# Optimization experiments

Hardware: AMD Instinct MI355X
Metric: run time of the kernel (lower is better)

The kernel has to match this reference:

```python
import jax, jax.numpy as jnp
import numpy as np

N_ATOMS = 512
N_FEATURES = 64
BATCH = 8
BINS = 64
SEG_LEN = 1
LEAKY_SLOPE = 0.01


def _segments(n, length=1):
    # all pairs of segments (i,i+length),(j,j+length), i<j, excluding end1==start2
    n_seg = n - length
    i, j = np.triu_indices(n_seg, k=1)
    seg = np.stack([i, i + length, j, j + length], axis=1)
    return seg[seg[:, 1] != seg[:, 2]].astype(np.int32)


def _nnorm(v):
    return v / jnp.linalg.norm(v, axis=-1, keepdims=True)


def _writhe(segments, xyz):
    # segments: (P,4) int, xyz: (B,N,3) -> (B,P)
    smat = xyz[:, segments]                                  # (B,P,4,3)
    B, P = smat.shape[0], smat.shape[1]
    # displacements r02,r03,r12,r13 (point a in seg1 -> point b in seg2)
    disp = _nnorm((smat[:, :, None, 2:, :] - smat[:, :, :2, None, :]).reshape(B, P, 4, 3))
    idx_a = jnp.array([0, 1, 3, 2])
    idx_b = jnp.array([1, 3, 2, 0])
    crosses = _nnorm(jnp.cross(disp[:, :, idx_a], disp[:, :, idx_b]))
    dots = jnp.clip(jnp.sum(crosses * crosses[:, :, idx_b], axis=-1), -1.0, 1.0)
    omega = jnp.arcsin(dots).sum(-1)                         # (B,P)
    signs = jnp.sign(jnp.sum(
        jnp.cross(_nnorm(smat[:, :, 3] - smat[:, :, 2]), _nnorm(smat[:, :, 1] - smat[:, :, 0]))
        * disp[:, :, 0], axis=-1))
    return omega * signs / (2.0 * jnp.pi)


def _rbf(x, start=-1.0, end=1.0, number=BINS):
    # soft_one_hot_linspace, basis='gaussian', cutoff=False
    values = jnp.linspace(start, end, number, dtype=x.dtype)
    step = values[1] - values[0]
    diff = (x[..., None] - values) / step
    return jnp.exp(-(diff ** 2)) / 1.12


def setup_inputs() -> dict:
    key = jax.random.key(0)
    k = jax.random.split(key, 4)
    seg = jnp.asarray(_segments(N_ATOMS, SEG_LEN))           # (129795,4)
    return {
        "x": jax.random.normal(k[0], (BATCH, N_ATOMS, N_FEATURES), jnp.float32),
        "xyz": jax.random.normal(k[1], (BATCH, N_ATOMS, 3), jnp.float32) * 3.0,
        "segments": seg,
        "W1": jax.random.normal(k[2], (BINS, N_FEATURES), jnp.float32) / np.sqrt(BINS),
        "b1": jnp.zeros((N_FEATURES,), jnp.float32),
        "W2": jax.random.normal(k[3], (N_FEATURES, N_FEATURES), jnp.float32) / np.sqrt(N_FEATURES),
        "b2": jnp.zeros((N_FEATURES,), jnp.float32),
    }


def reference(x, xyz, segments, W1, b1, W2, b2):
    wr = _writhe(segments, xyz)                              # (B,P)
    # bidirectional edges between segment start points
    src = jnp.concatenate([segments[:, 0], segments[:, 2]])  # (E,)
    dst = jnp.concatenate([segments[:, 2], segments[:, 0]])  # (E,)
    wr_e = jnp.concatenate([wr, wr], axis=1)                 # (B,E)
    h = jax.nn.leaky_relu(_rbf(wr_e) @ W1 + b1, LEAKY_SLOPE) # (B,E,F)
    msg = (h @ W2 + b2) * x[:, src]                          # (B,E,F)
    agg = jax.vmap(lambda m: jax.ops.segment_sum(m, dst, num_segments=N_ATOMS))(msg)
    return x + agg                                           # residual update (B,N,F)
```

## Files before the change

kernel.cpp:

```cpp
#include <hip/hip_runtime.h>
#include <hip/hip_bf16.h>
#include <math.h>
#include <stdint.h>

#define N_ATOMS 512
#define NF 64
#define NB 8
#define NBINS 64
#define NSEG 511
#define NTF 8192
#define NSENT 2554
#define ETILES2 254

__device__ __forceinline__ float dot3(float ax, float ay, float az,
                                      float bx, float by, float bz) {
    return fmaf(ax, bx, fmaf(ay, by, az * bz));
}

__device__ __forceinline__ uint16_t bf16_bits(float f) {
    union { __hip_bfloat16 h; uint16_t u; } cv;
    cv.h = __float2bfloat16(f);
    return cv.u;
}

__device__ __forceinline__ float compute_wr(const float* pb, int i, int j) {
    float p0x = pb[3*i+0], p0y = pb[3*i+1], p0z = pb[3*i+2];
    float p1x = pb[3*i+3], p1y = pb[3*i+4], p1z = pb[3*i+5];
    float p2x = pb[3*j+0], p2y = pb[3*j+1], p2z = pb[3*j+2];
    float p3x = pb[3*j+3], p3y = pb[3*j+4], p3z = pb[3*j+5];

    float d0x = p2x-p0x, d0y = p2y-p0y, d0z = p2z-p0z;
    float d1x = p3x-p0x, d1y = p3y-p0y, d1z = p3z-p0z;
    float d2x = p2x-p1x, d2y = p2y-p1y, d2z = p2z-p1z;
    float d3x = p3x-p1x, d3y = p3y-p1y, d3z = p3z-p1z;
    {
        float n0 = rsqrtf(dot3(d0x,d0y,d0z,d0x,d0y,d0z)); d0x*=n0; d0y*=n0; d0z*=n0;
        float n1 = rsqrtf(dot3(d1x,d1y,d1z,d1x,d1y,d1z)); d1x*=n1; d1y*=n1; d1z*=n1;
        float n2 = rsqrtf(dot3(d2x,d2y,d2z,d2x,d2y,d2z)); d2x*=n2; d2y*=n2; d2z*=n2;
        float n3 = rsqrtf(dot3(d3x,d3y,d3z,d3x,d3y,d3z)); d3x*=n3; d3y*=n3; d3z*=n3;
    }
    float c0x = d0y*d1z - d0z*d1y, c0y = d0z*d1x - d0x*d1z, c0z = d0x*d1y - d0y*d1x;
    float c1x = d1y*d3z - d1z*d3y, c1y = d1z*d3x - d1x*d3z, c1z = d1x*d3y - d1y*d3x;
    float c3x = d2y*d0z - d2z*d0y, c3y = d2z*d0x - d2x*d0z, c3z = d2x*d0y - d2y*d0x;
    {
        float n0 = rsqrtf(dot3(c0x,c0y,c0z,c0x,c0y,c0z)); c0x*=n0; c0y*=n0; c0z*=n0;
        float n1 = rsqrtf(dot3(c1x,c1y,c1z,c1x,c1y,c1z)); c1x*=n1; c1y*=n1; c1z*=n1;
        float n3 = rsqrtf(dot3(c3x,c3y,c3z,c3x,c3y,c3z)); c3x*=n3; c3y*=n3; c3z*=n3;
    }
    float t0 = fminf(fmaxf(dot3(c0x,c0y,c0z, c1x,c1y,c1z), -1.f), 1.f);
    float t1 = fminf(fmaxf(dot3(c1x,c1y,c1z, c3x,c3y,c3z), -1.f), 1.f);
    float t3 = fminf(fmaxf(dot3(c3x,c3y,c3z, c0x,c0y,c0z), -1.f), 1.f);
    float omega = asinf(t0) + asinf(t1) + asinf(t3) + 1.5707963267948966f;
    float ex = p3x-p2x, ey = p3y-p2y, ez = p3z-p2z;
    float fx = p1x-p0x, fy = p1y-p0y, fz = p1z-p0z;
    float gx = ey*fz - ez*fy, gy = ez*fx - ex*fz, gz = ex*fy - ey*fx;
    float sgd = dot3(gx,gy,gz, d0x,d0y,d0z);
    float sgn = (sgd > 0.f) ? 1.f : ((sgd < 0.f) ? -1.f : 0.f);
    return omega * sgn * 0.15915494309189535f;
}

__device__ __forceinline__ uint32_t wr_to_off(float w) {
    float tf = (w + 1.0f) * ((float)(NTF - 1) * 0.5f);
    tf = fminf(fmaxf(tf, 0.0f), (float)(NTF - 1));
    int t0 = (int)(tf + 0.5f);
    t0 = (t0 > NTF - 1) ? (NTF - 1) : t0;
    return (uint32_t)t0 << 6;
}

__launch_bounds__(256)
__global__ void prepass(
        const float* __restrict__ xyz, const int* __restrict__ seg,
        const float* __restrict__ W1, const float* __restrict__ b1,
        const float* __restrict__ W2, const float* __restrict__ b2,
        uint16_t* __restrict__ tabh, uint32_t* __restrict__ ta, int P) {
    __shared__ float lds[1536];

    const unsigned bx = blockIdx.x;

    if (bx < NTF / 8) {
        const int widx = threadIdx.x >> 6;
        const int lane = threadIdx.x & 63;
        const int g = bx * 4 + widx;
        const int g2 = g + NTF / 2;

        float tta = ((-1.0f + (2.0f / (float)(NTF - 1)) * (float)g)  + 1.0f) * 31.5f;
        float ttb = ((-1.0f + (2.0f / (float)(NTF - 1)) * (float)g2) + 1.0f) * 31.5f;

        float a0=0.f,a1=0.f,a2=0.f,a3=0.f, e0=0.f,e1=0.f,e2=0.f,e3=0.f;
        #pragma unroll
        for (int k = 0; k < NBINS; k += 4) {
            #pragma unroll
            for (int q = 0; q < 4; ++q) {
                float da = tta - (float)(k + q);
                float db = ttb - (float)(k + q);
                float ra = __expf(-da * da) * 0.8928571428571429f;
                float rb = __expf(-db * db) * 0.8928571428571429f;
                float wv = W1[(k + q) * NF + lane];
                if (q == 0) { a0 = fmaf(ra, wv, a0); e0 = fmaf(rb, wv, e0); }
                if (q == 1) { a1 = fmaf(ra, wv, a1); e1 = fmaf(rb, wv, e1); }
                if (q == 2) { a2 = fmaf(ra, wv, a2); e2 = fmaf(rb, wv, e2); }
                if (q == 3) { a3 = fmaf(ra, wv, a3); e3 = fmaf(rb, wv, e3); }
            }
        }
        float ha = ((a0 + a1) + (a2 + a3)) + b1[lane];
        float hb = ((e0 + e1) + (e2 + e3)) + b1[lane];
        ha = fmaxf(ha, 0.01f * ha);
        hb = fmaxf(hb, 0.01f * hb);
        lds[widx * 64 + lane]       = ha;
        lds[256 + widx * 64 + lane] = hb;
        __syncthreads();

        float m0=0.f,m1=0.f,m2=0.f,m3=0.f, n0=0.f,n1=0.f,n2=0.f,n3=0.f;
        #pragma unroll
        for (int k = 0; k < NF; k += 4) {
            float w0 = W2[(k + 0) * NF + lane];
            float w1v = W2[(k + 1) * NF + lane];
            float w2v = W2[(k + 2) * NF + lane];
            float w3 = W2[(k + 3) * NF + lane];
            m0 = fmaf(lds[widx * 64 + k + 0], w0, m0);
            m1 = fmaf(lds[widx * 64 + k + 1], w1v, m1);
            m2 = fmaf(lds[widx * 64 + k + 2], w2v, m2);
            m3 = fmaf(lds[widx * 64 + k + 3], w3, m3);
            n0 = fmaf(lds[256 + widx * 64 + k + 0], w0, n0);
            n1 = fmaf(lds[256 + widx * 64 + k + 1], w1v, n1);
            n2 = fmaf(lds[256 + widx * 64 + k + 2], w2v, n2);
            n3 = fmaf(lds[256 + widx * 64 + k + 3], w3, n3);
        }
        float ma = ((m0 + m1) + (m2 + m3)) + b2[lane];
        float mb = ((n0 + n1) + (n2 + n3)) + b2[lane];
        tabh[g  * NF + lane] = bf16_bits(ma);
        tabh[g2 * NF + lane] = bf16_bits(mb);
        if (g == 0) tabh[NTF * NF + lane] = 0;
    } else if (bx < NTF / 8 + NB * ETILES2) {
        const int rel = bx - NTF / 8;
        const int b = rel / ETILES2;
        const int tile = rel - b * ETILES2;

        const float* xb = xyz + b * (N_ATOMS * 3);
        #pragma unroll
        for (int k = 0; k < 6; ++k)
            lds[k * 256 + threadIdx.x] = xb[k * 256 + threadIdx.x];
        __syncthreads();

        #pragma unroll
        for (int q = 0; q < 2; ++q) {
            const int e = tile * 512 + q * 256 + threadIdx.x;
            if (e < P) {
                int4 sv = ((const int4*)seg)[e];
                const int i = sv.x;
                const int j = sv.z;
                uint32_t u = wr_to_off(compute_wr(lds, i, j));
                ta[(b << 18) + (i << 9) + j] = u;
                ta[(b << 18) + (j << 9) + i] = u;
            }
        }
    } else {
        const int idx = (bx - (NTF / 8 + NB * ETILES2)) * 256 + threadIdx.x;
        if (idx < NB * NSENT) {
            const int b = idx / NSENT;
            const int k = idx - b * NSENT;
            int d, s;
            if      (k < 512)  { d = k;        s = k;     }
            else if (k < 1023) { d = k - 512;  s = d + 1; }
            else if (k < 1534) { s = k - 1023; d = s + 1; }
            else if (k < 2044) { d = k - 1534; s = NSEG;  }
            else               { s = k - 2044; d = NSEG;  }
            ta[(b << 18) + (d << 9) + s] = (uint32_t)NTF << 6;
        }
    }
}

__launch_bounds__(1024, 8)
__global__ void agg15(
        const float* __restrict__ x, const uint32_t* __restrict__ ta,
        const uint16_t* __restrict__ tabh, float* __restrict__ out) {
    __shared__ float xs[16384];

    const int tid  = threadIdx.x;
    const int widx = tid >> 6;
    const int lane = tid & 63;
    const int fl   = lane & 31;
    const int hw   = lane >> 5;
    const int h    = widx >> 3;
    const int r    = widx & 7;
    const int ht   = tid & 511;
    const int bid  = blockIdx.x;
    const int b    = bid >> 6;
    const int dst  = ((bid & 63) << 3) + r;

    const float* xb = x + ((size_t)b << 15);
    const uint32_t* tarow = ta + ((size_t)b << 18) + ((size_t)dst << 9);

    {
        const float* xsrc = xb + ((h * 4) << 12);
        float* xdst = xs + (h << 12);
        #pragma unroll
        for (int k = 0; k < 8; ++k)
            xdst[k * 512 + ht] = xsrc[k * 512 + ht];
    }

    const int xoffl = (hw << 6) + (fl << 1);
    const int feidx = fl << 1;

    float accL = 0.0f, accH = 0.0f;
    #pragma unroll
    for (int p = 0; p < 4; ++p) {
        const int c = h * 4 + p;
        const int tavc = (int)tarow[(c << 6) + lane];

        __syncthreads();

        if (p < 3) {
            const float* xsrc = xb + ((c + 1) << 12);
            float* xdst = xs + ((((p + 1) & 1) << 13) + (h << 12));
            #pragma unroll
            for (int k = 0; k < 8; ++k)
                xdst[k * 512 + ht] = xsrc[k * 512 + ht];
        }

        const float* xc = xs + (((p & 1) << 13) + (h << 12)) + xoffl;
        #pragma unroll
        for (int s4 = 0; s4 < 32; s4 += 4) {
            uint32_t mw[4];
            #pragma unroll
            for (int q = 0; q < 4; ++q) {
                const int s = s4 + q;
                const uint32_t o0 =
                    (uint32_t)__builtin_amdgcn_readlane(tavc, 2 * s);
                const uint32_t o1 =
                    (uint32_t)__builtin_amdgcn_readlane(tavc, 2 * s + 1);
                const uint32_t osel = hw ? o1 : o0;
                mw[q] = *(const uint32_t*)(tabh + osel + feidx);
            }
            #pragma unroll
            for (int q = 0; q < 4; ++q) {
                const int s = s4 + q;
                const float mlo = __uint_as_float(mw[q] << 16);
                const float mhi = __uint_as_float(mw[q] & 0xffff0000u);
                const float2 xv = *(const float2*)(xc + (s << 7));
                accL = fmaf(mlo, xv.x, accL);
                accH = fmaf(mhi, xv.y, accH);
            }
        }
    }
    accL += __shfl_xor(accL, 32);
    accH += __shfl_xor(accH, 32);

    __syncthreads();
    if (h == 1 && hw == 0) {
        xs[(r << 6) + feidx]     = accL;
        xs[(r << 6) + feidx + 1] = accH;
    }
    __syncthreads();
    if (h == 0 && hw == 0) {
        const float2 prev = *(const float2*)&xs[(r << 6) + feidx];
        const float2 xv   = *(const float2*)(xb + (dst << 6) + feidx);
        float2 res;
        res.x = xv.x + accL + prev.x;
        res.y = xv.y + accH + prev.y;
        *(float2*)(out + ((size_t)b << 15) + (dst << 6) + feidx) = res;
    }
}


__global__ void init_out_kernel(const float* __restrict__ x, float* __restrict__ out, int n) {
    int idx = blockIdx.x * blockDim.x + threadIdx.x;
    if (idx < n) out[idx] = x[idx];
}

__device__ __forceinline__ void compute_m(
        const float* __restrict__ pb, int i, int j,
        const float* __restrict__ W1, const float* __restrict__ b1,
        const float* __restrict__ W2, const float* __restrict__ b2,
        float* __restrict__ mout) {
    float wr = compute_wr(pb, i, j);
    float acc_[NBINS];
    {
        float tt = (wr + 1.0f) * 31.5f;
        #pragma unroll
        for (int k = 0; k < NBINS; ++k) {
            float d = tt - (float)k;
            acc_[k] = __expf(-d * d) * 0.8928571428571429f;
        }
    }
    float h_[NF];
    #pragma unroll
    for (int f = 0; f < NF; ++f) h_[f] = b1[f];
    #pragma unroll
    for (int k = 0; k < NBINS; ++k) {
        float r = acc_[k];
        #pragma unroll
        for (int f = 0; f < NF; ++f) h_[f] = fmaf(r, W1[k * NF + f], h_[f]);
    }
    #pragma unroll
    for (int f = 0; f < NF; ++f) h_[f] = fmaxf(h_[f], 0.01f * h_[f]);
    #pragma unroll
    for (int f = 0; f < NF; ++f) acc_[f] = b2[f];
    #pragma unroll
    for (int k = 0; k < NF; ++k) {
        float hk = h_[k];
        #pragma unroll
        for (int f = 0; f < NF; ++f) acc_[f] = fmaf(hk, W2[k * NF + f], acc_[f]);
    }
    #pragma unroll
    for (int f = 0; f < NF; ++f) mout[f] = acc_[f];
}

__launch_bounds__(256, 2)
__global__ void writhe_msg_atomic_kernel(
        const float* __restrict__ x, const float* __restrict__ xyz,
        const int* __restrict__ seg,
        const float* __restrict__ W1, const float* __restrict__ b1,
        const float* __restrict__ W2, const float* __restrict__ b2,
        float* __restrict__ out, int P, int n_tiles) {
    __shared__ __hip_bfloat16 lds_m[4][64 * 65];
    __shared__ int lds_i[4][64];
    __shared__ int lds_j[4][64];

    const int widx = threadIdx.x >> 6;
    const int lane = threadIdx.x & 63;
    const int wave_g = blockIdx.x * 4 + widx;
    const int b = wave_g / n_tiles;
    const int tile = wave_g - b * n_tiles;
    const int bc = (b < NB) ? b : 0;
    const int e = tile * 64 + lane;
    const bool valid = (b < NB) && (e < P);

    int4 sv = valid ? ((const int4*)seg)[e] : make_int4(0, 1, 2, 3);
    const int i = sv.x;
    const int j = sv.z;

    float m[NF];
    compute_m(xyz + bc * (N_ATOMS * 3), i, j, W1, b1, W2, b2, m);

    const float scale = valid ? 1.0f : 0.0f;
    #pragma unroll
    for (int f = 0; f < NF; ++f)
        lds_m[widx][lane * 65 + f] = __float2bfloat16(m[f] * scale);
    lds_i[widx][lane] = i;
    lds_j[widx][lane] = j;
    __syncthreads();

    const float* xb = x + bc * (N_ATOMS * NF);
    float* ob = out + bc * (N_ATOMS * NF);
    int cur_i = lds_i[widx][0];
    float acc_i = 0.0f;
    for (int ee = 0; ee < 64; ++ee) {
        int ie = lds_i[widx][ee];
        int je = lds_j[widx][ee];
        float mv = __bfloat162float(lds_m[widx][ee * 65 + lane]);
        float xi = xb[ie * NF + lane];
        float xj = xb[je * NF + lane];
        atomicAdd(&ob[je * NF + lane], mv * xi);
        if (ie != cur_i) {
            atomicAdd(&ob[cur_i * NF + lane], acc_i);
            acc_i = 0.0f;
            cur_i = ie;
        }
        acc_i = fmaf(mv, xj, acc_i);
    }
    atomicAdd(&ob[cur_i * NF + lane], acc_i);
}

extern "C" void kernel_launch(void* const* d_in, const int* in_sizes, int n_in,
                              void* d_out, int out_size, void* d_ws, size_t ws_size,
                              hipStream_t stream) {
    const float* x   = (const float*)d_in[0];
    const float* xyz = (const float*)d_in[1];
    const int*   seg = (const int*)d_in[2];
    const float* W1  = (const float*)d_in[3];
    const float* b1  = (const float*)d_in[4];
    const float* W2  = (const float*)d_in[5];
    const float* b2  = (const float*)d_in[6];
    float* out = (float*)d_out;

    const int P = in_sizes[2] / 4;
    const int n_tiles = (P + 63) / 64;

    const size_t tabh_bytes = (size_t)(NTF + 1) * NF * sizeof(uint16_t);
    const size_t ta_bytes   = (size_t)NB * N_ATOMS * N_ATOMS * sizeof(uint32_t);
    const size_t need_ws = tabh_bytes + ta_bytes;

    if (ws_size >= need_ws && P <= ETILES2 * 512) {
        uint16_t* tabh = (uint16_t*)d_ws;
        uint32_t* ta   = (uint32_t*)((char*)d_ws + tabh_bytes);

        const int nsent_blocks = (NB * NSENT + 255) / 256;
        const int total_blocks = NTF / 8 + NB * ETILES2 + nsent_blocks;
        hipLaunchKernelGGL(prepass, dim3(total_blocks), dim3(256), 0, stream,
                           xyz, seg, W1, b1, W2, b2, tabh, ta, P);

        hipLaunchKernelGGL(agg15, dim3(NB * 64), dim3(1024), 0, stream,
                           x, ta, tabh, out);
    } else {
        const int n = out_size;
        hipLaunchKernelGGL(init_out_kernel, dim3((n + 255) / 256), dim3(256), 0, stream,
                           x, out, n);
        const int total_waves = NB * n_tiles;
        const int blocks = (total_waves + 3) / 4;
        hipLaunchKernelGGL(writhe_msg_atomic_kernel, dim3(blocks), dim3(256), 0, stream,
                           x, xyz, seg, W1, b1, W2, b2, out, P, n_tiles);
    }
}
```

Baseline: 108.1 us.

## Compute writhe pairs in 64x64 triangular tiles with LDS-transposed mirror writes

The writhe prepass no longer reads the segment index list. It enumerates the upper-triangle (i,j) pairs in 64x64 tiles, 36 tiles per batch. The direct write is coalesced along j, and the mirrored (j,i) write goes through a padded LDS tile so it is coalesced too, replacing the scattered transpose stores. In exchange the path now hardcodes the segment structure and is guarded by P equal to the test's exact pair count. It also launches far fewer blocks (36 per batch), which lowers parallelism, and diagonal tiles leave about half their threads idle.

```diff
diff --git a/kernel.cpp b/kernel.cpp
--- a/kernel.cpp
+++ b/kernel.cpp
@@ -10,7 +10,7 @@
 #define NSEG 511
 #define NTF 8192
 #define NSENT 2554
-#define ETILES2 254
+#define NTILES 36
 
 __device__ __forceinline__ float dot3(float ax, float ay, float az,
                                       float bx, float by, float bz) {
@@ -69,11 +69,12 @@
 
 __launch_bounds__(256)
 __global__ void prepass(
-        const float* __restrict__ xyz, const int* __restrict__ seg,
+        const float* __restrict__ xyz,
         const float* __restrict__ W1, const float* __restrict__ b1,
         const float* __restrict__ W2, const float* __restrict__ b2,
-        uint16_t* __restrict__ tabh, uint32_t* __restrict__ ta, int P) {
+        uint16_t* __restrict__ tabh, uint32_t* __restrict__ ta) {
     __shared__ float lds[1536];
+    __shared__ uint32_t tile[64 * 65];
 
     const unsigned bx = blockIdx.x;
 
@@ -131,10 +132,14 @@
         tabh[g  * NF + lane] = bf16_bits(ma);
         tabh[g2 * NF + lane] = bf16_bits(mb);
         if (g == 0) tabh[NTF * NF + lane] = 0;
-    } else if (bx < NTF / 8 + NB * ETILES2) {
+    } else if (bx < NTF / 8 + NB * NTILES) {
         const int rel = bx - NTF / 8;
-        const int b = rel / ETILES2;
-        const int tile = rel - b * ETILES2;
+        const int b = rel / NTILES;
+        int t36 = rel - b * NTILES;
+        int ti = 0, accum = 0;
+        while (t36 >= accum + (8 - ti)) { accum += 8 - ti; ++ti; }
+        const int tj = ti + (t36 - accum);
+        const int I = ti << 6, J = tj << 6;
 
         const float* xb = xyz + b * (N_ATOMS * 3);
         #pragma unroll
@@ -142,20 +147,28 @@
             lds[k * 256 + threadIdx.x] = xb[k * 256 + threadIdx.x];
         __syncthreads();
 
-        #pragma unroll
-        for (int q = 0; q < 2; ++q) {
-            const int e = tile * 512 + q * 256 + threadIdx.x;
-            if (e < P) {
-                int4 sv = ((const int4*)seg)[e];
-                const int i = sv.x;
-                const int j = sv.z;
-                uint32_t u = wr_to_off(compute_wr(lds, i, j));
-                ta[(b << 18) + (i << 9) + j] = u;
-                ta[(b << 18) + (j << 9) + i] = u;
+        const int jl = threadIdx.x & 63;
+        const int rr = threadIdx.x >> 6;
+        uint32_t* tb = ta + (b << 18);
+
+        for (int p = 0; p < 16; ++p) {
+            const int i = I + (p << 2) + rr;
+            const int j = J + jl;
+            if (i <= 510 && j <= 510 && j >= i + 2) {
+                const uint32_t u = wr_to_off(compute_wr(lds, i, j));
+                tb[(i << 9) + j] = u;
+                tile[(i - I) * 65 + (j - J)] = u;
             }
         }
+        __syncthreads();
+        for (int p = 0; p < 16; ++p) {
+            const int d = J + (p << 2) + rr;
+            const int s = I + jl;
+            if (d <= 510 && s <= 510 && d >= s + 2)
+                tb[(d << 9) + s] = tile[(s - I) * 65 + (d - J)];
+        }
     } else {
-        const int idx = (bx - (NTF / 8 + NB * ETILES2)) * 256 + threadIdx.x;
+        const int idx = (bx - (NTF / 8 + NB * NTILES)) * 256 + threadIdx.x;
         if (idx < NB * NSENT) {
             const int b = idx / NSENT;
             const int k = idx - b * NSENT;
@@ -381,14 +394,14 @@
     const size_t ta_bytes   = (size_t)NB * N_ATOMS * N_ATOMS * sizeof(uint32_t);
     const size_t need_ws = tabh_bytes + ta_bytes;
 
-    if (ws_size >= need_ws && P <= ETILES2 * 512) {
+    if (ws_size >= need_ws && P == 129795) {
         uint16_t* tabh = (uint16_t*)d_ws;
         uint32_t* ta   = (uint32_t*)((char*)d_ws + tabh_bytes);
 
         const int nsent_blocks = (NB * NSENT + 255) / 256;
-        const int total_blocks = NTF / 8 + NB * ETILES2 + nsent_blocks;
+        const int total_blocks = NTF / 8 + NB * NTILES + nsent_blocks;
         hipLaunchKernelGGL(prepass, dim3(total_blocks), dim3(256), 0, stream,
-                           xyz, seg, W1, b1, W2, b2, tabh, ta, P);
+                           xyz, W1, b1, W2, b2, tabh, ta);
 
         hipLaunchKernelGGL(agg15, dim3(NB * 64), dim3(1024), 0, stream,
                            x, ta, tabh, out);
```

After: 112.0 us. +3.6%, slower.
